# Kernel optimization log

Hardware: AMD Instinct MI355X
Metric: run time of the kernel (lower is better)

The kernel has to match this reference:

```python
import jax, jax.numpy as jnp
import numpy as np

ALPHA = 0.2          # LeakyReLU negative slope
N = 4096             # num nodes
E = 262144           # num edges (avg degree 64)
NFEAT = 512
NHID = 64
NHEAD = 8
NCLASS = 16
NEG_INF = -1e20


def setup_inputs() -> dict:
    key = jax.random.key(0)
    ks = jax.random.split(key, 8)
    features = jax.random.normal(ks[0], (N, NFEAT), dtype=jnp.float32)
    edge_list = jax.random.randint(ks[1], (2, E), 0, N, dtype=jnp.int64)
    # xavier-uniform-ish init scaled like gain=1.414
    W_heads = jax.random.normal(ks[2], (NHEAD, NFEAT, NHID), dtype=jnp.float32) * (1.414 / np.sqrt(NFEAT))
    a_heads = jax.random.normal(ks[3], (NHEAD, 2 * NHID, 1), dtype=jnp.float32) * 0.1
    b_heads = jnp.zeros((NHEAD, NHID), dtype=jnp.float32)
    W_out = jax.random.normal(ks[4], (NHEAD * NHID, NCLASS), dtype=jnp.float32) * (1.414 / np.sqrt(NHEAD * NHID))
    a_out = jax.random.normal(ks[5], (2 * NCLASS, 1), dtype=jnp.float32) * 0.1
    b_out = jnp.zeros((NCLASS,), dtype=jnp.float32)
    return {
        "features": features, "edge_list": edge_list,
        "W_heads": W_heads, "a_heads": a_heads, "b_heads": b_heads,
        "W_out": W_out, "a_out": a_out, "b_out": b_out,
    }


def _gatconv(x, src, tgt, W, a, b):
    # dropout layers are identity in eval mode
    h = x @ W                                             # [N, F_out]
    # edge scores: gather endpoints, concat, project, LeakyReLU
    a_input = jnp.concatenate([h[src], h[tgt]], axis=1)   # [E, 2*F_out]
    e = jax.nn.leaky_relu((a_input @ a)[:, 0], ALPHA)     # [E]
    n = h.shape[0]
    # dense NxN attention: -1e20 default, edge scores scattered in
    att = jnp.full((n, n), NEG_INF, dtype=h.dtype).at[src, tgt].set(e)
    att = jax.nn.softmax(att, axis=1)                     # rows w/o edges -> uniform (matches torch)
    return att @ h + b                                    # [N, F_out]


def reference(features, edge_list, W_heads, a_heads, b_heads, W_out, a_out, b_out):
    src, tgt = edge_list[0], edge_list[1]
    # multi-head GATConv, heads vmapped over stacked params -> [H, N, NHID]
    heads = jax.vmap(lambda W, a, b: _gatconv(features, src, tgt, W, a, b))(
        W_heads, a_heads, b_heads)
    # torch.cat over heads on dim=1 == transpose+reshape
    x = jnp.transpose(heads, (1, 0, 2)).reshape(N, NHEAD * NHID)
    x = jax.nn.elu(x)
    out = _gatconv(x, src, tgt, W_out, a_out, b_out)      # [N, NCLASS]
    return jax.nn.log_softmax(out, axis=1)
```

## Files before the change

kernel.cpp:

```cpp
#include <hip/hip_runtime.h>
#include <hip/hip_bf16.h>

#define NN 4096
#define NFEAT 512
#define NHID 64
#define NHEAD 8
#define NCLASS 16
#define CAP 160
#define LALPHA 0.2f

#define SZ2 (NHEAD*2*NHID)
#define SZ3 (NHEAD*NHID)
#define SZ4 (NFEAT*NCLASS)
#define SZ5 (2*NCLASS)
#define SZ6 (NCLASS)
#define NSMALL (SZ2+SZ3+SZ4+SZ5+SZ6)

typedef __attribute__((ext_vector_type(8))) short bf16x8;
typedef __attribute__((ext_vector_type(4))) float f32x4;
typedef __attribute__((ext_vector_type(8))) unsigned short u16x8;

__device__ __forceinline__ float b2f(unsigned short h) {
    return __uint_as_float(((unsigned int)h) << 16);
}
__device__ __forceinline__ unsigned short f2b(float f) {
    unsigned int u = __float_as_uint(f);
    unsigned int r = (u + 0x7fffu + ((u >> 16) & 1u)) >> 16;
    return (unsigned short)r;
}
__device__ __forceinline__ float waveMax(float v) {
#pragma unroll
    for (int m = 32; m >= 1; m >>= 1) v = fmaxf(v, __shfl_xor(v, m, 64));
    return v;
}
__device__ __forceinline__ float waveSum(float v) {
#pragma unroll
    for (int m = 32; m >= 1; m >>= 1) v += __shfl_xor(v, m, 64);
    return v;
}
__device__ __forceinline__ float lrelu(float e) {
    return e >= 0.f ? e : LALPHA * e;
}

__global__ void __launch_bounds__(256)
k_prep0(const void* __restrict__ f, const void* __restrict__ Wh_,
        const void* __restrict__ ah_, const void* __restrict__ bh_,
        const void* __restrict__ Wo_, const void* __restrict__ ao_,
        const void* __restrict__ bo_,
        unsigned short* __restrict__ featb,
        unsigned short* __restrict__ Wtb,
        float* __restrict__ smallf,
        unsigned int* __restrict__ bits,
        float* __restrict__ cmz) {
    int t = threadIdx.x, bid = blockIdx.x;
    for (int i = bid * 256 + t; i < NN * NN / 32; i += gridDim.x * 256)
        bits[i] = 0u;
    if (bid == 0)
        for (int i = t; i < NHEAD * NHID + NCLASS; i += 256) cmz[i] = 0.f;
    __shared__ int sbf;
    if (t < 64) {
        unsigned int w = ((const unsigned int*)f)[t];
        unsigned int lo = w & 0xffffu, e = (lo >> 7) & 0xffu;
        unsigned long long bal = __ballot(lo == 0u || (e >= 100u && e <= 140u));
        if (t == 0) sbf = (__popcll(bal) >= 40);
    }
    __syncthreads();
    bool bf = (sbf != 0);
    if (bid < 128) {
        __shared__ float tile[64][33];
        int h = bid >> 4, k0 = (bid & 15) * 32;
        int n = t & 63, kh = t >> 6;
#pragma unroll
        for (int i = 0; i < 8; ++i) {
            int kk = kh * 8 + i;
            int si = (h << 15) + (k0 + kk) * NHID + n;
            float v = bf ? b2f(((const unsigned short*)Wh_)[si])
                         : ((const float*)Wh_)[si];
            tile[n][kk] = v;
        }
        __syncthreads();
        int n2 = t >> 2, kk0 = (t & 3) * 8;
        u16x8 o;
#pragma unroll
        for (int i = 0; i < 8; ++i) o[i] = f2b(tile[n2][kk0 + i]);
        *(u16x8*)&Wtb[(size_t)((h << 6) + n2) * NFEAT + k0 + kk0] = o;
    } else {
        const int NF8 = NN * NFEAT / 8;
        int i = (bid - 128) * 256 + t;
        int stride = (gridDim.x - 128) * 256;
        const int TOT = NF8 + NSMALL;
        for (; i < TOT; i += stride) {
            if (i < NF8) {
                if (bf) {
                    *(u16x8*)&featb[i * 8] = ((const u16x8*)f)[i];
                } else {
                    float4 lo = ((const float4*)f)[i * 2];
                    float4 hi = ((const float4*)f)[i * 2 + 1];
                    u16x8 o;
                    o[0] = f2b(lo.x); o[1] = f2b(lo.y); o[2] = f2b(lo.z); o[3] = f2b(lo.w);
                    o[4] = f2b(hi.x); o[5] = f2b(hi.y); o[6] = f2b(hi.z); o[7] = f2b(hi.w);
                    *(u16x8*)&featb[i * 8] = o;
                }
            } else {
                int r = i - NF8;
                const void* sp; int off;
                if (r < SZ2)                        { sp = ah_; off = r; }
                else if (r < SZ2 + SZ3)             { sp = bh_; off = r - SZ2; }
                else if (r < SZ2 + SZ3 + SZ4)       { sp = Wo_; off = r - SZ2 - SZ3; }
                else if (r < SZ2 + SZ3 + SZ4 + SZ5) { sp = ao_; off = r - SZ2 - SZ3 - SZ4; }
                else                                { sp = bo_; off = r - SZ2 - SZ3 - SZ4 - SZ5; }
                smallf[r] = bf ? b2f(((const unsigned short*)sp)[off])
                               : ((const float*)sp)[off];
            }
        }
    }
}

__global__ void __launch_bounds__(256)
k_gemm_or(const unsigned short* __restrict__ Ab,
          const unsigned short* __restrict__ Wtb,
          const float* __restrict__ ah,
          unsigned short* __restrict__ Hb,
          float* __restrict__ s1, float* __restrict__ s2,
          float* __restrict__ cm1,
          const int* __restrict__ e32, int E,
          unsigned int* __restrict__ bits) {
    int t = threadIdx.x;
    if (blockIdx.x >= 256) {
        __shared__ int s64f;
        if (t < 64) {
            unsigned long long bal = __ballot(e32[2 * t + 1] == 0);
            if (t == 0) s64f = (__popcll(bal) >= 48);
        }
        __syncthreads();
        int i = (blockIdx.x - 256) * 256 + t;
        if (i < E) {
            int s, tt;
            if (s64f) { s = e32[2 * i]; tt = e32[2 * (E + i)]; }
            else      { s = e32[i];     tt = e32[E + i]; }
            s &= (NN - 1); tt &= (NN - 1);
            unsigned int pos = (unsigned int)s * NN + (unsigned int)tt;
            atomicOr(&bits[pos >> 5], 1u << (pos & 31u));
        }
        return;
    }
    __shared__ float cms[64];
    if (t < 64) cms[t] = 0.f;
    __syncthreads();
    int w = t >> 6, l = t & 63;
    int quad = l >> 4, l16 = l & 15;
    int h = blockIdx.x >> 5;
    int m0 = (blockIdx.x & 31) * 128 + w * 32;
    f32x4 acc[2][4] = {};
    const unsigned short* a0p = Ab + (size_t)(m0 + l16) * NFEAT + quad * 8;
    const unsigned short* a1p = a0p + 16 * NFEAT;
    const unsigned short* bp  = Wtb + ((size_t)h << 15) + (size_t)l16 * NFEAT + quad * 8;
#pragma unroll 4
    for (int k0 = 0; k0 < NFEAT; k0 += 32) {
        bf16x8 a0 = *(const bf16x8*)(a0p + k0);
        bf16x8 a1 = *(const bf16x8*)(a1p + k0);
#pragma unroll
        for (int nt = 0; nt < 4; ++nt) {
            bf16x8 b = *(const bf16x8*)(bp + (size_t)nt * 16 * NFEAT + k0);
            acc[0][nt] = __builtin_amdgcn_mfma_f32_16x16x32_bf16(a0, b, acc[0][nt], 0, 0, 0);
            acc[1][nt] = __builtin_amdgcn_mfma_f32_16x16x32_bf16(a1, b, acc[1][nt], 0, 0, 0);
        }
    }
    const float* av = ah + h * 2 * NHID;
    float p1[2][4] = {}, p2[2][4] = {};
#pragma unroll
    for (int rh = 0; rh < 2; ++rh) {
#pragma unroll
        for (int nt = 0; nt < 4; ++nt) {
            int col = nt * 16 + l16;
            float av1 = av[col], av2 = av[NHID + col];
            float csum = 0.f;
#pragma unroll
            for (int r = 0; r < 4; ++r) {
                float v = acc[rh][nt][r];
                int row = m0 + rh * 16 + quad * 4 + r;
                Hb[((size_t)row << 9) + (h << 6) + col] = f2b(v);
                p1[rh][r] += v * av1;
                p2[rh][r] += v * av2;
                csum += v;
            }
            atomicAdd(&cms[col], csum);
        }
    }
#pragma unroll
    for (int m = 8; m >= 1; m >>= 1)
#pragma unroll
        for (int rh = 0; rh < 2; ++rh)
#pragma unroll
            for (int r = 0; r < 4; ++r) {
                p1[rh][r] += __shfl_xor(p1[rh][r], m, 64);
                p2[rh][r] += __shfl_xor(p2[rh][r], m, 64);
            }
    if (l16 == 0) {
#pragma unroll
        for (int rh = 0; rh < 2; ++rh)
#pragma unroll
            for (int r = 0; r < 4; ++r) {
                int row = m0 + rh * 16 + quad * 4 + r;
                s1[(h << 12) + row] = p1[rh][r];
                s2[(h << 12) + row] = p2[rh][r];
            }
    }
    __syncthreads();
    if (t < 64) atomicAdd(&cm1[h * NHID + t], cms[t]);
}

__global__ void __launch_bounds__(256)
k_eattn1(const unsigned int* __restrict__ bits,
         int* __restrict__ deg, int* __restrict__ csr,
         const float* __restrict__ s1, const float* __restrict__ s2,
         const unsigned short* __restrict__ Hb,
         const float* __restrict__ bh, const float* __restrict__ cm1,
         const float* __restrict__ Wo, const float* __restrict__ ao,
         float* __restrict__ out2, float* __restrict__ s1o,
         float* __restrict__ s2o, float* __restrict__ cm2) {
    __shared__ float sW[4][CAP * 8];
    __shared__ int   sT[4][CAP];
    __shared__ float cms[NCLASS];
    int t = threadIdx.x;
    if (t < NCLASS) cms[t] = 0.f;
    int wid = t >> 6, lane = t & 63;
    int n = blockIdx.x * 4 + wid;
    int d;
    {
        uint2 w2 = *(const uint2*)&bits[n * 128 + lane * 2];
        int c = __popc(w2.x) + __popc(w2.y);
        int incl = c;
#pragma unroll
        for (int off = 1; off < 64; off <<= 1) {
            int u = __shfl_up(incl, off, 64);
            if (lane >= off) incl += u;
        }
        int excl = incl - c;
        int total = __shfl(incl, 63, 64);
        if (lane == 0) deg[n] = total;
        int tbase = lane * 64;
        unsigned int x = w2.x;
        while (x) {
            int b = __ffs(x) - 1; x &= x - 1;
            if (excl < CAP) sT[wid][excl] = tbase + b;
            ++excl;
        }
        unsigned int y = w2.y;
        while (y) {
            int b = __ffs(y) - 1; y &= y - 1;
            if (excl < CAP) sT[wid][excl] = tbase + 32 + b;
            ++excl;
        }
        d = min(total, CAP);
    }
    __syncthreads();
    for (int k = lane; k < d; k += 64) csr[(size_t)n * CAP + k] = sT[wid][k];
    int h = lane >> 3, jslot = lane & 7;
    float acc[8] = {};
    float rden = 1.f;
    if (d > 0) {
        const float* s2h = s2 + ((size_t)h << 12);
        float s1n = s1[(h << 12) + n];
        float mx = -1e30f;
        for (int jb = 0; jb < d; jb += 8) {
            int j = jb + jslot;
            int tt = (j < d) ? sT[wid][j] : 0;
            float e = (j < d) ? lrelu(s1n + s2h[tt]) : -1e30f;
            sW[wid][(j << 3) + h] = e;
            mx = fmaxf(mx, e);
        }
        mx = fmaxf(mx, __shfl_xor(mx, 1, 64));
        mx = fmaxf(mx, __shfl_xor(mx, 2, 64));
        mx = fmaxf(mx, __shfl_xor(mx, 4, 64));
        float den = 0.f;
        for (int jb = 0; jb < d; jb += 8) {
            int j = jb + jslot;
            float e = sW[wid][(j << 3) + h];
            float w = __expf(e - mx);
            sW[wid][(j << 3) + h] = w;
            den += w;
        }
        den += __shfl_xor(den, 1, 64);
        den += __shfl_xor(den, 2, 64);
        den += __shfl_xor(den, 4, 64);
        rden = 1.f / den;
        const unsigned short* Hp = Hb + lane * 8;
        int j = 0;
        for (; j + 4 <= d; j += 4) {
            int t0 = sT[wid][j],     t1 = sT[wid][j + 1];
            int t2 = sT[wid][j + 2], t3 = sT[wid][j + 3];
            float w0 = sW[wid][(j << 3) + h];
            float w1 = sW[wid][((j + 1) << 3) + h];
            float w2 = sW[wid][((j + 2) << 3) + h];
            float w3 = sW[wid][((j + 3) << 3) + h];
            u16x8 v0 = *(const u16x8*)(Hp + ((size_t)t0 << 9));
            u16x8 v1 = *(const u16x8*)(Hp + ((size_t)t1 << 9));
            u16x8 v2 = *(const u16x8*)(Hp + ((size_t)t2 << 9));
            u16x8 v3 = *(const u16x8*)(Hp + ((size_t)t3 << 9));
#pragma unroll
            for (int i = 0; i < 8; ++i)
                acc[i] += w0 * b2f(v0[i]) + w1 * b2f(v1[i])
                        + w2 * b2f(v2[i]) + w3 * b2f(v3[i]);
        }
        for (; j < d; ++j) {
            int t0 = sT[wid][j];
            float w0 = sW[wid][(j << 3) + h];
            u16x8 v0 = *(const u16x8*)(Hp + ((size_t)t0 << 9));
#pragma unroll
            for (int i = 0; i < 8; ++i) acc[i] += w0 * b2f(v0[i]);
        }
    }
    float o[8];
    if (d == 0) {
#pragma unroll
        for (int i = 0; i < 8; ++i) o[i] = cm1[lane * 8 + i] * (1.0f / NN);
    } else {
#pragma unroll
        for (int i = 0; i < 8; ++i) o[i] = acc[i] * rden;
    }
#pragma unroll
    for (int i = 0; i < 8; ++i) {
        float v = o[i] + bh[lane * 8 + i];
        o[i] = v > 0.f ? v : __expf(v) - 1.f;
    }
    float* xw = sW[wid];
    *(float4*)&xw[lane * 8]     = make_float4(o[0], o[1], o[2], o[3]);
    *(float4*)&xw[lane * 8 + 4] = make_float4(o[4], o[5], o[6], o[7]);
    int c = lane & 15, sub = lane >> 4;
    const float* xp = xw + sub * 128;
    const float* wp = Wo + sub * 128 * NCLASS + c;
    float a2 = 0.f;
#pragma unroll 8
    for (int kk = 0; kk < 128; ++kk) a2 += xp[kk] * wp[kk * NCLASS];
    a2 += __shfl_xor(a2, 16, 64);
    a2 += __shfl_xor(a2, 32, 64);
    if (lane < 16) out2[n * NCLASS + c] = a2;
    float r1 = a2 * ao[c], r2 = a2 * ao[NCLASS + c];
#pragma unroll
    for (int m = 8; m >= 1; m >>= 1) {
        r1 += __shfl_xor(r1, m, 16);
        r2 += __shfl_xor(r2, m, 16);
    }
    if (lane == 0) { s1o[n] = r1; s2o[n] = r2; }
    if (lane < 16) atomicAdd(&cms[c], a2);
    __syncthreads();
    if (t < NCLASS) atomicAdd(&cm2[t], cms[t]);
}

__global__ void __launch_bounds__(256)
k_attn2(const int* __restrict__ deg, const int* __restrict__ csr,
        const float* __restrict__ s1o, const float* __restrict__ s2o,
        const float* __restrict__ out2, const float* __restrict__ bo,
        const float* __restrict__ cm2, float* __restrict__ outp) {
    __shared__ float wv[4][CAP];
    __shared__ float o2s[4][16];
    int wid = threadIdx.x >> 6, lane = threadIdx.x & 63;
    int n = blockIdx.x * 4 + wid;
    int c = lane & 15;
    int d = min(deg[n], CAP);
    float val;
    if (d == 0) {
        val = cm2[c] * (1.0f / NN);
    } else {
        float s1n = s1o[n];
        const int* rowp = csr + (size_t)n * CAP;
        int t0 = (lane < d)       ? rowp[lane]       : 0;
        int t1 = (lane + 64 < d)  ? rowp[lane + 64]  : 0;
        int t2 = (lane + 128 < d) ? rowp[lane + 128] : 0;
        float e0 = (lane < d)       ? lrelu(s1n + s2o[t0]) : -1e30f;
        float e1 = (lane + 64 < d)  ? lrelu(s1n + s2o[t1]) : -1e30f;
        float e2 = (lane + 128 < d) ? lrelu(s1n + s2o[t2]) : -1e30f;
        float m = waveMax(fmaxf(e0, fmaxf(e1, e2)));
        float w0 = (lane < d)       ? __expf(e0 - m) : 0.f;
        float w1 = (lane + 64 < d)  ? __expf(e1 - m) : 0.f;
        float w2 = (lane + 128 < d) ? __expf(e2 - m) : 0.f;
        float den = waveSum(w0 + w1 + w2);
        wv[wid][lane] = w0;
        if (lane + 64 < CAP)  wv[wid][lane + 64]  = w1;
        if (lane + 128 < CAP) wv[wid][lane + 128] = w2;
        int g2 = lane >> 2, q = lane & 3;
        float a4[4] = {};
        for (int j = g2; j < d; j += 16) {
            float w = wv[wid][j];
            int tt = rowp[j];
            float4 v = *(const float4*)(out2 + tt * NCLASS + q * 4);
            a4[0] += w * v.x; a4[1] += w * v.y;
            a4[2] += w * v.z; a4[3] += w * v.w;
        }
#pragma unroll
        for (int m2 = 4; m2 <= 32; m2 <<= 1)
#pragma unroll
            for (int i = 0; i < 4; ++i) a4[i] += __shfl_xor(a4[i], m2, 64);
        if (lane < 4)
            *(float4*)&o2s[wid][lane * 4] = make_float4(a4[0], a4[1], a4[2], a4[3]);
        val = o2s[wid][c] / den;
    }
    val += bo[c];
    float mx = val;
#pragma unroll
    for (int m = 8; m >= 1; m >>= 1) mx = fmaxf(mx, __shfl_xor(mx, m, 16));
    float se = __expf(val - mx);
#pragma unroll
    for (int m = 8; m >= 1; m >>= 1) se += __shfl_xor(se, m, 16);
    float res = val - mx - __logf(se);
    if (lane < 16) outp[n * NCLASS + lane] = res;
}

extern "C" void kernel_launch(void* const* d_in, const int* in_sizes, int n_in,
                              void* d_out, int out_size, void* d_ws, size_t ws_size,
                              hipStream_t stream) {
    const void* features = d_in[0];
    const int*  edges    = (const int*)d_in[1];
    const void* W_heads  = d_in[2];
    const void* a_heads  = d_in[3];
    const void* b_heads  = d_in[4];
    const void* W_out    = d_in[5];
    const void* a_out    = d_in[6];
    const void* b_out    = d_in[7];
    int E = in_sizes[1] / 2;
    int csb = (E + 255) / 256;

    unsigned int* bits = (unsigned int*)d_ws;
    int*   deg  = (int*)(bits + (NN * NN / 32));
    float* cm1  = (float*)(deg + NN);
    float* cm2  = cm1 + NHEAD * NHID;
    int*   csr  = (int*)(cm2 + NCLASS);
    float* s1   = (float*)(csr + NN * CAP);
    float* s2   = s1 + NHEAD * NN;
    float* out2 = s2 + NHEAD * NN;
    float* s1o  = out2 + NN * NCLASS;
    float* s2o  = s1o + NN;
    float* smallf = s2o + NN;
    unsigned short* Hb    = (unsigned short*)(smallf + NSMALL);
    unsigned short* featb = Hb + (size_t)NN * NHEAD * NHID;
    unsigned short* Wtb   = featb + (size_t)NN * NFEAT;
    float* outp = (float*)d_out;

    hipLaunchKernelGGL(k_prep0, dim3(2048), dim3(256), 0, stream,
                       features, W_heads, a_heads, b_heads, W_out, a_out, b_out,
                       featb, Wtb, smallf, bits, cm1);
    hipLaunchKernelGGL(k_gemm_or, dim3(256 + csb), dim3(256), 0, stream,
                       featb, Wtb, smallf, Hb, s1, s2, cm1, edges, E, bits);
    hipLaunchKernelGGL(k_eattn1, dim3(NN / 4), dim3(256), 0, stream,
                       bits, deg, csr, s1, s2, Hb, smallf + SZ2, cm1,
                       smallf + SZ2 + SZ3, smallf + SZ2 + SZ3 + SZ4,
                       out2, s1o, s2o, cm2);
    hipLaunchKernelGGL(k_attn2, dim3(NN / 4), dim3(256), 0, stream,
                       deg, csr, s1o, s2o, out2,
                       smallf + SZ2 + SZ3 + SZ4 + SZ5, cm2, outp);
}
```

Measured before the change: 143.7 us.

## Read bf16 features directly in GEMM and widen gather unroll to eight

When the input features are already bf16, the prep kernel no longer copies them into a staging buffer. The GEMM kernel instead runs its own heuristic dtype check and reads the features in place. Separately, the neighbour aggregation loop in the first attention kernel is unrolled from four to eight edges so more gather loads are in flight at once. This trades a duplicated dtype heuristic and higher register pressure for less memory traffic and more latency hiding.

```diff
diff --git a/kernel.cpp b/kernel.cpp
--- a/kernel.cpp
+++ b/kernel.cpp
@@ -86,21 +86,17 @@
         *(u16x8*)&Wtb[(size_t)((h << 6) + n2) * NFEAT + k0 + kk0] = o;
     } else {
         const int NF8 = NN * NFEAT / 8;
-        int i = (bid - 128) * 256 + t;
+        const int TOT = NF8 + NSMALL;
         int stride = (gridDim.x - 128) * 256;
-        const int TOT = NF8 + NSMALL;
-        for (; i < TOT; i += stride) {
+        int start = bf ? NF8 : 0;
+        for (int i = start + (bid - 128) * 256 + t; i < TOT; i += stride) {
             if (i < NF8) {
-                if (bf) {
-                    *(u16x8*)&featb[i * 8] = ((const u16x8*)f)[i];
-                } else {
-                    float4 lo = ((const float4*)f)[i * 2];
-                    float4 hi = ((const float4*)f)[i * 2 + 1];
-                    u16x8 o;
-                    o[0] = f2b(lo.x); o[1] = f2b(lo.y); o[2] = f2b(lo.z); o[3] = f2b(lo.w);
-                    o[4] = f2b(hi.x); o[5] = f2b(hi.y); o[6] = f2b(hi.z); o[7] = f2b(hi.w);
-                    *(u16x8*)&featb[i * 8] = o;
-                }
+                float4 lo = ((const float4*)f)[i * 2];
+                float4 hi = ((const float4*)f)[i * 2 + 1];
+                u16x8 o;
+                o[0] = f2b(lo.x); o[1] = f2b(lo.y); o[2] = f2b(lo.z); o[3] = f2b(lo.w);
+                o[4] = f2b(hi.x); o[5] = f2b(hi.y); o[6] = f2b(hi.z); o[7] = f2b(hi.w);
+                *(u16x8*)&featb[i * 8] = o;
             } else {
                 int r = i - NF8;
                 const void* sp; int off;
@@ -117,7 +113,8 @@
 }
 
 __global__ void __launch_bounds__(256)
-k_gemm_or(const unsigned short* __restrict__ Ab,
+k_gemm_or(const void* __restrict__ f,
+          const unsigned short* __restrict__ featb,
           const unsigned short* __restrict__ Wtb,
           const float* __restrict__ ah,
           unsigned short* __restrict__ Hb,
@@ -144,9 +141,17 @@
         }
         return;
     }
+    __shared__ int sbf;
+    if (t < 64) {
+        unsigned int w = ((const unsigned int*)f)[t];
+        unsigned int lo = w & 0xffffu, e = (lo >> 7) & 0xffu;
+        unsigned long long bal = __ballot(lo == 0u || (e >= 100u && e <= 140u));
+        if (t == 0) sbf = (__popcll(bal) >= 40);
+    }
     __shared__ float cms[64];
     if (t < 64) cms[t] = 0.f;
     __syncthreads();
+    const unsigned short* Ab = sbf ? (const unsigned short*)f : featb;
     int w = t >> 6, l = t & 63;
     int quad = l >> 4, l16 = l & 15;
     int h = blockIdx.x >> 5;
@@ -287,21 +292,22 @@
         rden = 1.f / den;
         const unsigned short* Hp = Hb + lane * 8;
         int j = 0;
-        for (; j + 4 <= d; j += 4) {
-            int t0 = sT[wid][j],     t1 = sT[wid][j + 1];
-            int t2 = sT[wid][j + 2], t3 = sT[wid][j + 3];
-            float w0 = sW[wid][(j << 3) + h];
-            float w1 = sW[wid][((j + 1) << 3) + h];
-            float w2 = sW[wid][((j + 2) << 3) + h];
-            float w3 = sW[wid][((j + 3) << 3) + h];
-            u16x8 v0 = *(const u16x8*)(Hp + ((size_t)t0 << 9));
-            u16x8 v1 = *(const u16x8*)(Hp + ((size_t)t1 << 9));
-            u16x8 v2 = *(const u16x8*)(Hp + ((size_t)t2 << 9));
-            u16x8 v3 = *(const u16x8*)(Hp + ((size_t)t3 << 9));
-#pragma unroll
-            for (int i = 0; i < 8; ++i)
-                acc[i] += w0 * b2f(v0[i]) + w1 * b2f(v1[i])
-                        + w2 * b2f(v2[i]) + w3 * b2f(v3[i]);
+        for (; j + 8 <= d; j += 8) {
+            int tt[8]; float ww[8];
+#pragma unroll
+            for (int q = 0; q < 8; ++q) {
+                tt[q] = sT[wid][j + q];
+                ww[q] = sW[wid][((j + q) << 3) + h];
+            }
+            u16x8 vv[8];
+#pragma unroll
+            for (int q = 0; q < 8; ++q)
+                vv[q] = *(const u16x8*)(Hp + ((size_t)tt[q] << 9));
+#pragma unroll
+            for (int q = 0; q < 8; ++q)
+#pragma unroll
+                for (int i = 0; i < 8; ++i)
+                    acc[i] += ww[q] * b2f(vv[q][i]);
         }
         for (; j < d; ++j) {
             int t0 = sT[wid][j];
@@ -441,7 +447,7 @@
                        features, W_heads, a_heads, b_heads, W_out, a_out, b_out,
                        featb, Wtb, smallf, bits, cm1);
     hipLaunchKernelGGL(k_gemm_or, dim3(256 + csb), dim3(256), 0, stream,
-                       featb, Wtb, smallf, Hb, s1, s2, cm1, edges, E, bits);
+                       features, featb, Wtb, smallf, Hb, s1, s2, cm1, edges, E, bits);
     hipLaunchKernelGGL(k_eattn1, dim3(NN / 4), dim3(256), 0, stream,
                        bits, deg, csr, s1, s2, Hb, smallf + SZ2, cm1,
                        smallf + SZ2 + SZ3, smallf + SZ2 + SZ3 + SZ4,
```

After: 142.3 us. No clear change (-1.0%).
